# Optimization experiments

Hardware: AMD Instinct MI355X
Metric: run time of the kernel (lower is better)

The kernel has to match this reference:

```python
import jax, jax.numpy as jnp
import numpy as np

NB, NLOC, NALL, NNEI = 1, 4096, 6144, 64
N_EDGE, N_ANGLE, A_SEL = 262144, 409600, 10
N_DIM, E_DIM, A_DIM, AXIS = 128, 64, 32, 4
SEL_REDUCE = 10.0


def _lin_params(key, din, dout):
    k1, k2 = jax.random.split(key)
    W = jax.random.normal(k1, (din, dout), jnp.float32) / np.float32(np.sqrt(din))
    b = jax.random.normal(k2, (dout,), jnp.float32) * 0.01
    return W, b


def setup_inputs():
    key = jax.random.key(0)
    ks = jax.random.split(key, 20)
    inp = {}
    inp["node_ebd_ext"] = jax.random.normal(ks[0], (NB, NALL, N_DIM), jnp.float32)
    inp["edge_ebd"] = jax.random.normal(ks[1], (N_EDGE, E_DIM), jnp.float32)
    inp["h2"] = jax.random.normal(ks[2], (N_EDGE, 3), jnp.float32)
    inp["angle_ebd"] = jax.random.normal(ks[3], (N_ANGLE, A_DIM), jnp.float32)
    inp["nlist"] = jax.random.randint(ks[4], (NB, NLOC, NNEI), 0, NALL)
    inp["nlist_mask"] = jnp.ones((NB, NLOC, NNEI), jnp.bool_)
    inp["sw"] = jax.random.uniform(ks[5], (N_EDGE,), jnp.float32)
    inp["a_nlist"] = jax.random.randint(ks[6], (NB, NLOC, A_SEL), 0, NALL)
    inp["a_nlist_mask"] = jnp.ones((NB, NLOC, A_SEL), jnp.bool_)
    inp["a_sw"] = jax.random.uniform(ks[7], (N_ANGLE,), jnp.float32)
    n2e = jax.random.randint(ks[8], (N_EDGE,), 0, NB * NLOC)
    n_ext2e = jax.random.randint(ks[9], (N_EDGE,), 0, NB * NALL)
    inp["edge_index"] = jnp.stack([n2e, n_ext2e])
    n2a = jax.random.randint(ks[10], (N_ANGLE,), 0, NB * NLOC)
    eij2a = jax.random.randint(ks[11], (N_ANGLE,), 0, N_EDGE)
    eik2a = jax.random.randint(ks[12], (N_ANGLE,), 0, N_EDGE)
    inp["angle_index"] = jnp.stack([n2a, eij2a, eik2a])
    sym_dim = (N_DIM + E_DIM) * AXIS          # 768
    edge_info_dim = 2 * N_DIM + E_DIM         # 320
    angle_dim = A_DIM + N_DIM + 2 * E_DIM     # 288
    inp["W_node_self"], inp["b_node_self"] = _lin_params(ks[13], N_DIM, N_DIM)
    inp["W_node_sym"], inp["b_node_sym"] = _lin_params(ks[14], sym_dim, N_DIM)
    inp["W_node_edge"], inp["b_node_edge"] = _lin_params(ks[15], edge_info_dim, N_DIM)
    inp["W_edge_self"], inp["b_edge_self"] = _lin_params(ks[16], edge_info_dim, E_DIM)
    inp["W_edge_angle1"], inp["b_edge_angle1"] = _lin_params(ks[17], angle_dim, E_DIM)
    inp["W_edge_angle2"], inp["b_edge_angle2"] = _lin_params(ks[18], E_DIM, E_DIM)
    inp["W_angle_self"], inp["b_angle_self"] = _lin_params(ks[19], angle_dim, A_DIM)
    inp["n_res0"] = jnp.full((N_DIM,), 0.1, jnp.float32)
    inp["n_res1"] = jnp.full((N_DIM,), 0.1, jnp.float32)
    inp["n_res2"] = jnp.full((N_DIM,), 0.1, jnp.float32)
    inp["e_res0"] = jnp.full((E_DIM,), 0.1, jnp.float32)
    inp["e_res1"] = jnp.full((E_DIM,), 0.1, jnp.float32)
    inp["a_res0"] = jnp.full((A_DIM,), 0.1, jnp.float32)
    return inp


def reference(node_ebd_ext, edge_ebd, h2, angle_ebd, nlist, nlist_mask, sw,
              a_nlist, a_nlist_mask, a_sw, edge_index, angle_index,
              W_node_self, b_node_self, W_node_sym, b_node_sym,
              W_node_edge, b_node_edge, W_edge_self, b_edge_self,
              W_edge_angle1, b_edge_angle1, W_edge_angle2, b_edge_angle2,
              W_angle_self, b_angle_self,
              n_res0, n_res1, n_res2, e_res0, e_res1, a_res0):
    act = jax.nn.silu
    nb, nloc, nnei = nlist.shape
    n_dim = node_ebd_ext.shape[-1]
    n_edge = h2.shape[0]
    dyn_e_sel = nnei / SEL_REDUCE
    dyn_a_sel = a_nlist.shape[-1] / SEL_REDUCE
    node_ebd = node_ebd_ext[:, :nloc]
    n2e, n_ext2e = edge_index[0], edge_index[1]
    n2a, eij2a, eik2a = angle_index[0], angle_index[1], angle_index[2]
    nei_node_ebd = node_ebd_ext.reshape(-1, n_dim)[n_ext2e]  # [n_edge, n_dim]
    node_self = act(node_ebd @ W_node_self + b_node_self)

    def sym_op(flat_ebd):
        # symmetrization: outer(h2, sw*ebd) scattered to owners, then grrg
        d = flat_ebd.shape[-1]
        w = flat_ebd * sw[:, None]
        h2g2 = jax.ops.segment_sum(
            (h2[:, :, None] * w[:, None, :]).reshape(n_edge, 3 * d),
            n2e, num_segments=nb * nloc)
        h2g2 = h2g2.reshape(nb, nloc, 3, d) * (dyn_e_sel ** -0.5)
        m = h2g2[..., :AXIS]  # [nb, nloc, 3, axis]
        g = jnp.einsum('blxa,blxd->blad', m, h2g2) / 3.0
        return g.reshape(nb, nloc, AXIS * d)

    sym_edge = sym_op(edge_ebd)
    sym_node = sym_op(nei_node_ebd)
    node_sym = act(jnp.concatenate([sym_edge, sym_node], -1) @ W_node_sym + b_node_sym)
    node_i = node_ebd.reshape(-1, n_dim)[n2e]
    edge_info = jnp.concatenate([node_i, nei_node_ebd, edge_ebd], -1)  # [n_edge, 320]
    node_edge_update = act(edge_info @ W_node_edge + b_node_edge) * sw[:, None]
    node_edge_msg = jax.ops.segment_sum(node_edge_update, n2e, num_segments=nb * nloc).reshape(nb, nloc, -1) / dyn_e_sel
    n_updated = node_ebd + n_res0 * node_self + n_res1 * node_sym + n_res2 * node_edge_msg
    edge_self = act(edge_info @ W_edge_self + b_edge_self)
    node_for_angle = node_ebd.reshape(-1, n_dim)[n2a]
    edge_ik = edge_ebd[eik2a]
    edge_ij = edge_ebd[eij2a]
    angle_info = jnp.concatenate([angle_ebd, node_for_angle, edge_ik, edge_ij], -1)  # [n_angle, 288]
    edge_angle = act(angle_info @ W_edge_angle1 + b_edge_angle1)
    reduced = jax.ops.segment_sum(edge_angle * a_sw[:, None], eij2a, num_segments=n_edge) / (dyn_a_sel ** 0.5)
    edge_angle_msg = act(reduced @ W_edge_angle2 + b_edge_angle2)
    e_updated = edge_ebd + e_res0 * edge_self + e_res1 * edge_angle_msg
    angle_self = act(angle_info @ W_angle_self + b_angle_self)
    a_updated = angle_ebd + a_res0 * angle_self
    return (n_updated, e_updated, a_updated)
```

## Files before the change

### kernel.cpp

```cpp
#include <hip/hip_runtime.h>
#include <hip/hip_bf16.h>

#define NLOC_   4096
#define NALL_   6144
#define NEDGE_  262144
#define NANGLE_ 409600

typedef __bf16 bf16x8 __attribute__((ext_vector_type(8)));
typedef float  f32x4  __attribute__((ext_vector_type(4)));
typedef unsigned short u16;

__device__ __forceinline__ float silu_(float x){ return x / (1.0f + __expf(-x)); }

__device__ __forceinline__ u16 f2bu(float f){
    union { float f; unsigned u; } v; v.f = f;
    unsigned r = v.u + 0x7fffu + ((v.u >> 16) & 1u);
    return (u16)(r >> 16);
}
__device__ __forceinline__ float bu2f(u16 b){
    union { unsigned u; float f; } v; v.u = ((unsigned)b) << 16; return v.f;
}
__device__ __forceinline__ void st_bf16x4(u16* dst, float4 v){
    unsigned lo = (unsigned)f2bu(v.x) | ((unsigned)f2bu(v.y) << 16);
    unsigned hi = (unsigned)f2bu(v.z) | ((unsigned)f2bu(v.w) << 16);
    *reinterpret_cast<uint2*>(dst) = make_uint2(lo, hi);
}

__global__ __launch_bounds__(256) void k_mega_prep(
    const float* __restrict__ Wne, const float* __restrict__ Wes,
    const float* __restrict__ W1,  const float* __restrict__ WA,
    const float* __restrict__ W2,  const float* __restrict__ Wsym,
    const float* __restrict__ Wns,
    const float* __restrict__ node_ext, const float* __restrict__ edge_ebd,
    const float* __restrict__ angle_ebd,
    const int* __restrict__ n2e, const int* __restrict__ eij2a,
    u16* __restrict__ WTe, u16* __restrict__ WTa, u16* __restrict__ WT2,
    u16* __restrict__ WsymT, u16* __restrict__ WnsT,
    u16* __restrict__ NB, u16* __restrict__ EB, u16* __restrict__ AB,
    int* __restrict__ cnt, int* __restrict__ cnt2)
{
    const int b = blockIdx.x, tid = threadIdx.x;
    if (b < 812) {
        int i = b*256 + tid;
        if (i < 61440) {
            int r = i/320, c = i - r*320;
            WTe[i] = f2bu(r < 128 ? Wne[c*128 + r] : Wes[c*64 + (r-128)]);
        } else if (i < 89088) {
            int j = i - 61440; int r = j/288, c = j - r*288;
            WTa[j] = f2bu(r < 64 ? W1[c*64 + r] : WA[c*32 + (r-64)]);
        } else if (i < 93184) {
            int j = i - 89088; int r = j >> 6, c = j & 63;
            WT2[j] = f2bu(W2[c*64 + r]);
        } else if (i < 191488) {
            int j = i - 93184; int r = j/768, c = j - r*768;
            WsymT[j] = f2bu(Wsym[c*128 + r]);
        } else {
            int j = i - 191488; int r = j >> 7, c = j & 127;
            WnsT[j] = f2bu(Wns[c*128 + r]);
        }
    } else if (b < 1580) {
        int i = (b - 812)*256 + tid;
        float4 v = ((const float4*)node_ext)[i];
        st_bf16x4(&NB[(size_t)i*4], v);
    } else if (b < 3628) {
        for (int i = (b - 1580)*256 + tid; i < NEDGE_*64/4; i += 2048*256) {
            float4 v = ((const float4*)edge_ebd)[i];
            st_bf16x4(&EB[(size_t)i*4], v);
        }
    } else if (b < 5676) {
        for (int i = (b - 3628)*256 + tid; i < NANGLE_*32/4; i += 2048*256) {
            float4 v = ((const float4*)angle_ebd)[i];
            st_bf16x4(&AB[(size_t)i*4], v);
        }
    } else if (b < 6700) {
        int e = (b - 5676)*256 + tid;
        atomicAdd(&cnt[n2e[e]], 1);
    } else {
        int a = (b - 6700)*256 + tid;
        atomicAdd(&cnt2[eij2a[a]], 1);
    }
}

__global__ __launch_bounds__(256) void k_scan_misc(
    const int* __restrict__ cnt, int* __restrict__ off, int* __restrict__ cursor,
    const int* __restrict__ cnt2, int* __restrict__ bsum,
    const u16* __restrict__ NB, const u16* __restrict__ WTe,
    float* __restrict__ nconst)
{
    __shared__ __align__(16) u16 sN[64][136];
    int* wa = (int*)&sN[0][0];
    const int b = blockIdx.x, t = threadIdx.x;

    if (b == 0) {
        int v[16]; int s = 0;
        #pragma unroll
        for (int k = 0; k < 16; ++k) { v[k] = s; s += cnt[16*t + k]; }
        wa[t] = s;
        __syncthreads();
        for (int d = 1; d < 256; d <<= 1) {
            int x = wa[t];
            int y = (t >= d) ? wa[t-d] : 0;
            __syncthreads();
            wa[t] = x + y;
            __syncthreads();
        }
        int excl = (t == 0) ? 0 : wa[t-1];
        #pragma unroll
        for (int k = 0; k < 16; ++k) {
            off[16*t + k]    = excl + v[k];
            cursor[16*t + k] = excl + v[k];
        }
        if (t == 255) off[4096] = excl + s;
    } else if (b <= 256) {
        int bb = b - 1;
        int4 v = ((const int4*)cnt2)[bb*256 + t];
        wa[t] = v.x + v.y + v.z + v.w;
        __syncthreads();
        for (int d = 128; d > 0; d >>= 1) {
            if (t < d) wa[t] += wa[t+d];
            __syncthreads();
        }
        if (t == 0) bsum[bb] = wa[0];
    } else {
        const int e0 = (b - 257) * 64;
        #pragma unroll
        for (int f = t; f < 1024; f += 256) {
            int r = f >> 4, c = f & 15;
            *(uint4*)&sN[r][8*c] = ((const uint4*)&NB[(size_t)(e0 + r)*128])[c];
        }
        __syncthreads();
        const int w = t >> 6, l = t & 63;
        const int lr = l & 15, hq = l >> 4, lk = hq * 8;
        f32x4 acc[4][3] = {};
        #pragma unroll
        for (int kk = 0; kk < 4; ++kk) {
            bf16x8 a[4], bb[3];
            #pragma unroll
            for (int m = 0; m < 4; ++m)
                a[m] = *(const bf16x8*)&sN[16*m + lr][kk*32 + lk];
            #pragma unroll
            for (int nf = 0; nf < 3; ++nf)
                bb[nf] = *(const bf16x8*)&WTe[(size_t)(48*w + 16*nf + lr)*320 + kk*32 + lk];
            #pragma unroll
            for (int m = 0; m < 4; ++m)
                #pragma unroll
                for (int nf = 0; nf < 3; ++nf)
                    acc[m][nf] = __builtin_amdgcn_mfma_f32_16x16x32_bf16(a[m], bb[nf], acc[m][nf], 0, 0, 0);
        }
        #pragma unroll
        for (int nf = 0; nf < 3; ++nf) {
            int c = 48*w + 16*nf + lr;
            #pragma unroll
            for (int m = 0; m < 4; ++m)
                #pragma unroll
                for (int j = 0; j < 4; ++j) {
                    int r = 16*m + 4*hq + j;
                    nconst[(size_t)(e0 + r)*192 + c] = acc[m][nf][j];
                }
        }
    }
}

__global__ void k_scan2b(const int* __restrict__ bsum, int* __restrict__ boff)
{
    __shared__ int wa[256];
    int t = threadIdx.x;
    wa[t] = bsum[t];
    __syncthreads();
    for (int d = 1; d < 256; d <<= 1) {
        int x = wa[t];
        int y = (t >= d) ? wa[t-d] : 0;
        __syncthreads();
        wa[t] = x + y;
        __syncthreads();
    }
    boff[t] = (t == 0) ? 0 : wa[t-1];
}

__global__ void k_scan2c(const int* __restrict__ cnt2, const int* __restrict__ boff,
                         int* __restrict__ off2, int* __restrict__ cursor2)
{
    __shared__ int wa[256];
    int b = blockIdx.x, t = threadIdx.x;
    int4 v = ((const int4*)cnt2)[b*256 + t];
    int s1 = v.x, s2 = s1 + v.y, s3 = s2 + v.z, s4 = s3 + v.w;
    wa[t] = s4;
    __syncthreads();
    for (int d = 1; d < 256; d <<= 1) {
        int x = wa[t];
        int y = (t >= d) ? wa[t-d] : 0;
        __syncthreads();
        wa[t] = x + y;
        __syncthreads();
    }
    int base = boff[b] + ((t == 0) ? 0 : wa[t-1]);
    int i = (b*256 + t)*4;
    off2[i]   = base;      cursor2[i]   = base;
    off2[i+1] = base + s1; cursor2[i+1] = base + s1;
    off2[i+2] = base + s2; cursor2[i+2] = base + s2;
    off2[i+3] = base + s3; cursor2[i+3] = base + s3;
    if (b == 255 && t == 255) off2[NEDGE_] = NANGLE_;
}

__global__ void k_fill2(const int* __restrict__ n2e, int* __restrict__ cursor,
                        int* __restrict__ csr,
                        const int* __restrict__ eij2a, int* __restrict__ cursor2,
                        int* __restrict__ rank2)
{
    int b = blockIdx.x;
    if (b < 1024) {
        int e = b*256 + threadIdx.x;
        int pos = atomicAdd(&cursor[n2e[e]], 1);
        csr[pos] = e;
    } else {
        int a = (b - 1024)*256 + threadIdx.x;
        int pos = atomicAdd(&cursor2[eij2a[a]], 1);
        rank2[a] = pos;
    }
}

__global__ __launch_bounds__(256, 4) void k_edge_flat(
    const u16* __restrict__ NB, const u16* __restrict__ EB,
    const float* __restrict__ h2, const float* __restrict__ sw,
    const int* __restrict__ n2e, const int* __restrict__ n_ext2e,
    const int* __restrict__ csr,
    const u16* __restrict__ WTe, const float* __restrict__ nconst,
    const float* __restrict__ bne, const float* __restrict__ bes,
    float* __restrict__ msg,
    float* __restrict__ h2g2_e, float* __restrict__ h2g2_n,
    u16* __restrict__ eselfO)
{
    __shared__ __align__(16) u16 sA[64][200];
    __shared__ float sH[4][576];
    __shared__ int   s_eid[64];
    __shared__ int   s_node[64];
    __shared__ int   s_g[64];
    __shared__ float s_sw[64];
    __shared__ float s_h2[64][3];
    __shared__ int   s_segstart[65];
    __shared__ int   s_nseg;

    const int tid = threadIdx.x;
    const int w  = tid >> 6, l = tid & 63;
    const int lr = l & 15, hq = l >> 4, lk = hq * 8;
    const int base = blockIdx.x * 64;

    if (tid < 64) {
        int e = csr[base + tid];
        s_eid[tid]  = e;
        s_node[tid] = n2e[e];
        s_g[tid]    = n_ext2e[e];
        s_sw[tid]   = sw[e];
        s_h2[tid][0] = h2[e*3];
        s_h2[tid][1] = h2[e*3+1];
        s_h2[tid][2] = h2[e*3+2];
    }
    __syncthreads();

    if (tid < 64) {
        bool flag = (tid == 0) || (s_node[tid] != s_node[tid-1]);
        unsigned long long mask = __ballot(flag);
        if (flag) {
            int sid = __popcll(mask & ((1ull << tid) - 1ull));
            s_segstart[sid] = tid;
        }
        if (tid == 0) {
            int ns = __popcll(mask);
            s_nseg = ns;
            s_segstart[ns] = 64;
        }
    }

    #pragma unroll
    for (int f = tid; f < 1024; f += 256) {
        int r = f >> 4, c = f & 15;
        *(uint4*)&sA[r][8*c] = ((const uint4*)&NB[(size_t)s_g[r]*128])[c];
    }
    #pragma unroll
    for (int f = tid; f < 512; f += 256) {
        int r = f >> 3, c = f & 7;
        *(uint4*)&sA[r][128 + 8*c] = ((const uint4*)&EB[(size_t)s_eid[r]*64])[c];
    }
    __syncthreads();

    float bias[3];
    int   cful[3];
    #pragma unroll
    for (int nf = 0; nf < 3; ++nf) {
        int c = 48*w + 16*nf + lr;
        cful[nf] = c;
        bias[nf] = (c < 128) ? bne[c] : bes[c-128];
    }

    f32x4 acc[4][3] = {};
    #pragma unroll
    for (int kk = 0; kk < 6; ++kk) {
        bf16x8 a[4], b[3];
        #pragma unroll
        for (int m = 0; m < 4; ++m)
            a[m] = *(const bf16x8*)&sA[16*m + lr][kk*32 + lk];
        #pragma unroll
        for (int nf = 0; nf < 3; ++nf)
            b[nf] = *(const bf16x8*)&WTe[(size_t)cful[nf]*320 + 128 + kk*32 + lk];
        #pragma unroll
        for (int m = 0; m < 4; ++m)
            #pragma unroll
            for (int nf = 0; nf < 3; ++nf)
                acc[m][nf] = __builtin_amdgcn_mfma_f32_16x16x32_bf16(a[m], b[nf], acc[m][nf], 0, 0, 0);
    }

    #pragma unroll
    for (int nf = 0; nf < 3; ++nf) {
        int c = cful[nf];
        if (c < 128) {
            #pragma unroll
            for (int m = 0; m < 4; ++m)
                #pragma unroll
                for (int j = 0; j < 4; ++j) {
                    int r = 16*m + 4*hq + j;
                    float ncv = nconst[(size_t)s_node[r]*192 + c];
                    acc[m][nf][j] = silu_(acc[m][nf][j] + ncv + bias[nf]) * s_sw[r];
                }
        } else {
            int c2 = c - 128;
            #pragma unroll
            for (int m = 0; m < 4; ++m)
                #pragma unroll
                for (int j = 0; j < 4; ++j) {
                    int r = 16*m + 4*hq + j;
                    float ncv = nconst[(size_t)s_node[r]*192 + c];
                    eselfO[(size_t)s_eid[r]*64 + c2] =
                        f2bu(silu_(acc[m][nf][j] + ncv + bias[nf]));
                }
        }
    }

    const int nseg = s_nseg;
    for (int s = 0; s < nseg; ++s) {
        int rs = s_segstart[s], re = s_segstart[s+1];
        int nd = s_node[rs];
        #pragma unroll
        for (int nf = 0; nf < 3; ++nf) {
            if (cful[nf] >= 128) continue;
            float v = 0.f;
            #pragma unroll
            for (int m = 0; m < 4; ++m)
                #pragma unroll
                for (int j = 0; j < 4; ++j) {
                    int r = 16*m + 4*hq + j;
                    v += (r >= rs && r < re) ? acc[m][nf][j] : 0.f;
                }
            v += __shfl_xor(v, 16);
            v += __shfl_xor(v, 32);
            if (hq == 0) atomicAdd(&msg[(size_t)nd*128 + cful[nf]], v);
        }
    }

    for (int s = 0; s < nseg; ++s) {
        int rs = s_segstart[s], re = s_segstart[s+1];
        int nd = s_node[rs];
        int lo = max(16*w, rs), hi = min(16*w + 16, re);
        float hacc[9] = {0.f,0.f,0.f,0.f,0.f,0.f,0.f,0.f,0.f};
        for (int r = lo; r < hi; ++r) {
            float swv = s_sw[r];
            float s0 = s_h2[r][0] * swv;
            float s1 = s_h2[r][1] * swv;
            float s2 = s_h2[r][2] * swv;
            float eb = bu2f(sA[r][128 + l]);
            float n0 = bu2f(sA[r][l]);
            float n1 = bu2f(sA[r][64 + l]);
            hacc[0] = fmaf(s0, eb, hacc[0]);
            hacc[1] = fmaf(s1, eb, hacc[1]);
            hacc[2] = fmaf(s2, eb, hacc[2]);
            hacc[3] = fmaf(s0, n0, hacc[3]);
            hacc[4] = fmaf(s0, n1, hacc[4]);
            hacc[5] = fmaf(s1, n0, hacc[5]);
            hacc[6] = fmaf(s1, n1, hacc[6]);
            hacc[7] = fmaf(s2, n0, hacc[7]);
            hacc[8] = fmaf(s2, n1, hacc[8]);
        }
        #pragma unroll
        for (int q = 0; q < 3; ++q) sH[w][q*64 + l] = hacc[q];
        #pragma unroll
        for (int q = 0; q < 6; ++q) sH[w][192 + q*64 + l] = hacc[3+q];
        __syncthreads();
        for (int i = tid; i < 576; i += 256) {
            float v = sH[0][i] + sH[1][i] + sH[2][i] + sH[3][i];
            if (i < 192) atomicAdd(&h2g2_e[(size_t)nd*192 + i], v);
            else         atomicAdd(&h2g2_n[(size_t)nd*384 + (i - 192)], v);
        }
        __syncthreads();
    }
}

__global__ __launch_bounds__(256) void k_angle_mfma(
    const u16* __restrict__ NB, const u16* __restrict__ EB,
    const u16* __restrict__ AB, const float* __restrict__ a_sw,
    const int* __restrict__ n2a, const int* __restrict__ eij2a,
    const int* __restrict__ eik2a, const int* __restrict__ rank2,
    const u16* __restrict__ WTa,
    const float* __restrict__ b1, const float* __restrict__ bA,
    const float* __restrict__ a_res0,
    u16* __restrict__ ea, float* __restrict__ a_out)
{
    __shared__ __align__(16) u16 sA[32][296];
    __shared__ __align__(16) u16 sEA[32][64];
    __shared__ int s_na[32], s_ij[32], s_ik[32], s_rk[32];
    __shared__ float s_asw[32];
    const int tid = threadIdx.x;
    const int a0 = blockIdx.x * 32;

    if (tid < 32) {
        s_na[tid] = n2a[a0 + tid];
        s_ij[tid] = eij2a[a0 + tid];
        s_ik[tid] = eik2a[a0 + tid];
        s_rk[tid] = rank2[a0 + tid];
        s_asw[tid] = a_sw[a0 + tid];
    }
    __syncthreads();

    if (tid < 128) {
        int r = tid >> 2, c = tid & 3;
        *(uint4*)&sA[r][8*c] = ((const uint4*)&AB[(size_t)(a0 + r)*32])[c];
    }
    #pragma unroll
    for (int f = tid; f < 512; f += 256) {
        int r = f >> 4, c = f & 15;
        *(uint4*)&sA[r][32 + 8*c] = ((const uint4*)&NB[(size_t)s_na[r]*128])[c];
    }
    {
        int r = tid >> 3, c = tid & 7;
        *(uint4*)&sA[r][160 + 8*c] = ((const uint4*)&EB[(size_t)s_ik[r]*64])[c];
        *(uint4*)&sA[r][224 + 8*c] = ((const uint4*)&EB[(size_t)s_ij[r]*64])[c];
    }
    __syncthreads();

    const int w = tid >> 6, l = tid & 63;
    const int lr = l & 15, hq = l >> 4, lk = hq * 8;
    const int mrow  = (w & 1) * 16;
    const int nbase = (w >> 1) * 48;

    f32x4 acc[3] = {};
    #pragma unroll
    for (int kk = 0; kk < 9; ++kk) {
        bf16x8 a = *(const bf16x8*)&sA[mrow + lr][kk*32 + lk];
        #pragma unroll
        for (int nf = 0; nf < 3; ++nf) {
            bf16x8 b = *(const bf16x8*)&WTa[(size_t)(nbase + 16*nf + lr)*288 + kk*32 + lk];
            acc[nf] = __builtin_amdgcn_mfma_f32_16x16x32_bf16(a, b, acc[nf], 0, 0, 0);
        }
    }

    #pragma unroll
    for (int nf = 0; nf < 3; ++nf) {
        int c = nbase + 16*nf + lr;
        if (c < 64) {
            float bb = b1[c];
            #pragma unroll
            for (int j = 0; j < 4; ++j) {
                int r = mrow + 4*hq + j;
                sEA[r][c] = f2bu(silu_(acc[nf][j] + bb) * s_asw[r]);
            }
        } else {
            int c2 = c - 64;
            float bb = bA[c2], rr = a_res0[c2];
            #pragma unroll
            for (int j = 0; j < 4; ++j) {
                int r = mrow + 4*hq + j;
                size_t idx = (size_t)(a0 + r)*32 + c2;
                a_out[idx] = bu2f(sA[r][c2]) + rr * silu_(acc[nf][j] + bb);
            }
        }
    }
    __syncthreads();

    {
        int r = tid >> 3, c = tid & 7;
        *(uint4*)&ea[(size_t)s_rk[r]*64 + 8*c] = *(const uint4*)&sEA[r][8*c];
    }
}

__global__ __launch_bounds__(256) void k_fin(
    const u16* __restrict__ EB, const u16* __restrict__ eselfO,
    const u16* __restrict__ ea, const int* __restrict__ off2,
    const u16* __restrict__ WT2,
    const float* __restrict__ b2_, const float* __restrict__ er0,
    const float* __restrict__ er1,
    float* __restrict__ e_out,
    const float* __restrict__ h2g2_e, const float* __restrict__ h2g2_n,
    u16* __restrict__ symcB)
{
    __shared__ __align__(16) u16 sR[64][72];
    __shared__ __align__(16) u16 sE[64][72];
    __shared__ __align__(16) u16 sB[64][72];
    const int tid = threadIdx.x;
    const int blk = blockIdx.x;

    if (blk < 4096) {
        const int e0 = blk * 64;
        const int w = tid >> 6, l = tid & 63;

        #pragma unroll
        for (int f = tid; f < 512; f += 256) {
            int r = f >> 3, c = f & 7;
            *(uint4*)&sB[r][8*c] = ((const uint4*)&EB[(size_t)(e0 + r)*64])[c];
            *(uint4*)&sE[r][8*c] = ((const uint4*)&eselfO[(size_t)(e0 + r)*64])[c];
        }

        #pragma unroll
        for (int r16 = 0; r16 < 16; ++r16) {
            int r = w*16 + r16;
            int e = e0 + r;
            float s = 0.f;
            int jb = off2[e], je = off2[e+1];
            for (int j = jb; j < je; ++j)
                s += bu2f(ea[(size_t)j*64 + l]);
            sR[r][l] = f2bu(s);
        }
        __syncthreads();

        const int lr = l & 15, hq = l >> 4, lk = hq * 8;
        f32x4 acc[4] = {};
        #pragma unroll
        for (int kk = 0; kk < 2; ++kk) {
            bf16x8 b = *(const bf16x8*)&WT2[(size_t)(16*w + lr)*64 + kk*32 + lk];
            #pragma unroll
            for (int m = 0; m < 4; ++m) {
                bf16x8 a = *(const bf16x8*)&sR[16*m + lr][kk*32 + lk];
                acc[m] = __builtin_amdgcn_mfma_f32_16x16x32_bf16(a, b, acc[m], 0, 0, 0);
            }
        }
        int c = 16*w + lr;
        float bb = b2_[c], r0 = er0[c], r1 = er1[c];
        #pragma unroll
        for (int m = 0; m < 4; ++m)
            #pragma unroll
            for (int j = 0; j < 4; ++j) {
                int r = 16*m + 4*hq + j;
                size_t idx = (size_t)(e0 + r)*64 + c;
                e_out[idx] = bu2f(sB[r][c]) + r0 * bu2f(sE[r][c])
                           + r1 * silu_(acc[m][j] + bb);
            }
    } else {
        const int n = blk - 4096;
        float* he = (float*)&sR[0][0];
        float* hn = he + 192;
        for (int i = tid; i < 192; i += 256) he[i] = h2g2_e[(size_t)n*192 + i];
        for (int i = tid; i < 384; i += 256) hn[i] = h2g2_n[(size_t)n*384 + i];
        __syncthreads();
        const float SCALE = 1.0f / (6.4f * 3.0f);
        for (int i = tid; i < 768; i += 256) {
            float s;
            if (i < 256) {
                int a = i >> 6, j = i & 63;
                s = he[a]*he[j] + he[64+a]*he[64+j] + he[128+a]*he[128+j];
            } else {
                int i2 = i - 256;
                int a = i2 >> 7, j = i2 & 127;
                s = hn[a]*hn[j] + hn[128+a]*hn[128+j] + hn[256+a]*hn[256+j];
            }
            symcB[(size_t)n*768 + i] = f2bu(s * SCALE);
        }
    }
}

__global__ __launch_bounds__(256) void k_node_mfma(
    const u16* __restrict__ symcB, const u16* __restrict__ NB,
    const float* __restrict__ node_ext, const float* __restrict__ msg,
    const u16* __restrict__ WsymT, const u16* __restrict__ WnsT,
    const float* __restrict__ bns, const float* __restrict__ bsym,
    const float* __restrict__ nr0, const float* __restrict__ nr1,
    const float* __restrict__ nr2,
    float* __restrict__ n_out)
{
    __shared__ __align__(16) u16 sA[32][264];
    const int tid = threadIdx.x;
    const int n0 = blockIdx.x * 32;
    const int w = tid >> 6, l = tid & 63;
    const int lr = l & 15, hq = l >> 4, lk = hq * 8;

    f32x4 accY[2][2] = {};
    f32x4 accS[2][2] = {};

    for (int chunk = 0; chunk < 3; ++chunk) {
        __syncthreads();
        #pragma unroll
        for (int f = tid; f < 1024; f += 256) {
            int r = f >> 5, c = f & 31;
            *(uint4*)&sA[r][8*c] =
                ((const uint4*)&symcB[(size_t)(n0 + r)*768 + chunk*256])[c];
        }
        __syncthreads();
        #pragma unroll
        for (int kk = 0; kk < 8; ++kk) {
            bf16x8 a[2], b[2];
            #pragma unroll
            for (int m = 0; m < 2; ++m)
                a[m] = *(const bf16x8*)&sA[16*m + lr][kk*32 + lk];
            #pragma unroll
            for (int nf = 0; nf < 2; ++nf)
                b[nf] = *(const bf16x8*)&WsymT[(size_t)(32*w + 16*nf + lr)*768
                                               + chunk*256 + kk*32 + lk];
            #pragma unroll
            for (int m = 0; m < 2; ++m)
                #pragma unroll
                for (int nf = 0; nf < 2; ++nf)
                    accY[m][nf] = __builtin_amdgcn_mfma_f32_16x16x32_bf16(a[m], b[nf], accY[m][nf], 0, 0, 0);
        }
    }

    __syncthreads();
    #pragma unroll
    for (int f = tid; f < 512; f += 256) {
        int r = f >> 4, c = f & 15;
        *(uint4*)&sA[r][8*c] = ((const uint4*)&NB[(size_t)(n0 + r)*128])[c];
    }
    __syncthreads();
    #pragma unroll
    for (int kk = 0; kk < 4; ++kk) {
        bf16x8 a[2], b[2];
        #pragma unroll
        for (int m = 0; m < 2; ++m)
            a[m] = *(const bf16x8*)&sA[16*m + lr][kk*32 + lk];
        #pragma unroll
        for (int nf = 0; nf < 2; ++nf)
            b[nf] = *(const bf16x8*)&WnsT[(size_t)(32*w + 16*nf + lr)*128 + kk*32 + lk];
        #pragma unroll
        for (int m = 0; m < 2; ++m)
            #pragma unroll
            for (int nf = 0; nf < 2; ++nf)
                accS[m][nf] = __builtin_amdgcn_mfma_f32_16x16x32_bf16(a[m], b[nf], accS[m][nf], 0, 0, 0);
    }

    #pragma unroll
    for (int nf = 0; nf < 2; ++nf) {
        int c = 32*w + 16*nf + lr;
        float bS = bns[c], bY = bsym[c];
        float r0 = nr0[c], r1 = nr1[c], r2 = nr2[c];
        #pragma unroll
        for (int m = 0; m < 2; ++m)
            #pragma unroll
            for (int j = 0; j < 4; ++j) {
                int r = 16*m + 4*hq + j;
                size_t idx = (size_t)(n0 + r)*128 + c;
                float self_ = silu_(accS[m][nf][j] + bS);
                float sym_  = silu_(accY[m][nf][j] + bY);
                n_out[idx] = node_ext[idx] + r0*self_ + r1*sym_
                           + r2 * msg[idx] * (1.0f / 6.4f);
            }
    }
}

extern "C" void kernel_launch(void* const* d_in, const int* in_sizes, int n_in,
                              void* d_out, int out_size, void* d_ws, size_t ws_size,
                              hipStream_t stream)
{
    const float* node_ext  = (const float*)d_in[0];
    const float* edge_ebd  = (const float*)d_in[1];
    const float* h2        = (const float*)d_in[2];
    const float* angle_ebd = (const float*)d_in[3];
    const float* sw        = (const float*)d_in[6];
    const float* a_sw      = (const float*)d_in[9];
    const int*  edge_index  = (const int*)d_in[10];
    const int*  angle_index = (const int*)d_in[11];
    const int* n2e     = edge_index;
    const int* n_ext2e = edge_index + NEDGE_;
    const int* n2a     = angle_index;
    const int* eij2a   = angle_index + NANGLE_;
    const int* eik2a   = angle_index + 2*NANGLE_;

    const float* Wns  = (const float*)d_in[12];
    const float* bns  = (const float*)d_in[13];
    const float* Wsym = (const float*)d_in[14];
    const float* bsym = (const float*)d_in[15];
    const float* Wne  = (const float*)d_in[16];
    const float* bne  = (const float*)d_in[17];
    const float* Wes  = (const float*)d_in[18];
    const float* bes  = (const float*)d_in[19];
    const float* W1   = (const float*)d_in[20];
    const float* b1   = (const float*)d_in[21];
    const float* W2   = (const float*)d_in[22];
    const float* b2_  = (const float*)d_in[23];
    const float* WA   = (const float*)d_in[24];
    const float* bA   = (const float*)d_in[25];
    const float* nr0  = (const float*)d_in[26];
    const float* nr1  = (const float*)d_in[27];
    const float* nr2  = (const float*)d_in[28];
    const float* er0  = (const float*)d_in[29];
    const float* er1  = (const float*)d_in[30];
    const float* ar0  = (const float*)d_in[31];

    char* wsp = (char*)d_ws;
    u16*   ea      = (u16*)wsp;    wsp += (size_t)NANGLE_ * 64 * 2;
    u16*   EB      = (u16*)wsp;    wsp += (size_t)NEDGE_ * 64 * 2;
    u16*   NB      = (u16*)wsp;    wsp += (size_t)NALL_ * 128 * 2;
    u16*   AB      = (u16*)wsp;    wsp += (size_t)NANGLE_ * 32 * 2;
    u16*   eselfO  = (u16*)wsp;    wsp += (size_t)NEDGE_ * 64 * 2;
    u16*   symcB   = (u16*)wsp;    wsp += (size_t)NLOC_ * 768 * 2;
    int*   cnt     = (int*)wsp;    wsp += 4096 * 4;
    int*   cnt2    = (int*)wsp;    wsp += (size_t)NEDGE_ * 4;
    float* msg     = (float*)wsp;  wsp += (size_t)NLOC_ * 128 * 4;
    float* h2g2_e  = (float*)wsp;  wsp += (size_t)NLOC_ * 192 * 4;
    float* h2g2_n  = (float*)wsp;  wsp += (size_t)NLOC_ * 384 * 4;
    size_t zero_bytes = 4096*4 + (size_t)NEDGE_*4 + (size_t)NLOC_*128*4
                      + (size_t)NLOC_*192*4 + (size_t)NLOC_*384*4;
    int*   off     = (int*)wsp;    wsp += 4104 * 4;
    int*   cursor  = (int*)wsp;    wsp += 4096 * 4;
    int*   csr     = (int*)wsp;    wsp += (size_t)NEDGE_ * 4;
    int*   off2    = (int*)wsp;    wsp += ((size_t)NEDGE_ + 16) * 4;
    int*   cursor2 = (int*)wsp;    wsp += (size_t)NEDGE_ * 4;
    int*   bsum    = (int*)wsp;    wsp += 256 * 4;
    int*   boff    = (int*)wsp;    wsp += 256 * 4;
    int*   rank2   = (int*)wsp;    wsp += (size_t)NANGLE_ * 4;
    float* nconst  = (float*)wsp;  wsp += (size_t)NLOC_ * 192 * 4;
    u16*   WTe     = (u16*)wsp;    wsp += 192 * 320 * 2;
    u16*   WTa     = (u16*)wsp;    wsp += 96 * 288 * 2;
    u16*   WT2     = (u16*)wsp;    wsp += 64 * 64 * 2;
    u16*   WsymT   = (u16*)wsp;    wsp += 128 * 768 * 2;
    u16*   WnsT    = (u16*)wsp;    wsp += 128 * 128 * 2;

    hipMemsetAsync(cnt, 0, zero_bytes, stream);

    float* n_out = (float*)d_out;
    float* e_out = n_out + (size_t)NLOC_ * 128;
    float* a_out = e_out + (size_t)NEDGE_ * 64;

    k_mega_prep <<<8300, 256, 0, stream>>>(Wne, Wes, W1, WA, W2, Wsym, Wns,
                                           node_ext, edge_ebd, angle_ebd,
                                           n2e, eij2a,
                                           WTe, WTa, WT2, WsymT, WnsT,
                                           NB, EB, AB, cnt, cnt2);
    k_scan_misc <<<321, 256, 0, stream>>>(cnt, off, cursor, cnt2, bsum,
                                          NB, WTe, nconst);
    k_scan2b <<<1, 256, 0, stream>>>(bsum, boff);
    k_scan2c <<<256, 256, 0, stream>>>(cnt2, boff, off2, cursor2);
    k_fill2  <<<2624, 256, 0, stream>>>(n2e, cursor, csr, eij2a, cursor2, rank2);

    k_edge_flat <<<NEDGE_/64, 256, 0, stream>>>(NB, EB, h2, sw, n2e, n_ext2e, csr,
                                                WTe, nconst, bne, bes,
                                                msg, h2g2_e, h2g2_n, eselfO);
    k_angle_mfma <<<NANGLE_/32, 256, 0, stream>>>(NB, EB, AB, a_sw,
                                                  n2a, eij2a, eik2a, rank2,
                                                  WTa, b1, bA, ar0, ea, a_out);
    k_fin <<<8192, 256, 0, stream>>>(EB, eselfO, ea, off2, WT2, b2_, er0, er1,
                                     e_out, h2g2_e, h2g2_n, symcB);
    k_node_mfma <<<NLOC_/32, 256, 0, stream>>>(symcB, NB, node_ext, msg,
                                               WsymT, WnsT, bns, bsym,
                                               nr0, nr1, nr2, n_out);
}
```

Measured before the change: 423.8 us.

## Precompute per-node angle projection and iterate angles in CSR-sorted order

The node part of the angle linear layer (node_for_angle @ W[32:160]) is now computed once per local node (4096x96) in the scan kernel and stored in nconstA. The angle kernel then only gathers the angle and edge features (K=160 instead of 288) and adds the per-node constant before the activation. Angles are also processed in eij-sorted CSR order, so the ea stores become contiguous, but the angle_ebd reads and a_out writes are now scattered. This trades the per-angle 128-wide node gather and its MFMA work for an extra small GEMM and per-element gathers of nconstA.

```diff
diff --git a/kernel.cpp b/kernel.cpp
--- a/kernel.cpp
+++ b/kernel.cpp
@@ -34,8 +34,8 @@
     const float* __restrict__ node_ext, const float* __restrict__ edge_ebd,
     const float* __restrict__ angle_ebd,
     const int* __restrict__ n2e, const int* __restrict__ eij2a,
-    u16* __restrict__ WTe, u16* __restrict__ WTa, u16* __restrict__ WT2,
-    u16* __restrict__ WsymT, u16* __restrict__ WnsT,
+    u16* __restrict__ WTe, u16* __restrict__ WTa2, u16* __restrict__ WTaN,
+    u16* __restrict__ WT2, u16* __restrict__ WsymT, u16* __restrict__ WnsT,
     u16* __restrict__ NB, u16* __restrict__ EB, u16* __restrict__ AB,
     int* __restrict__ cnt, int* __restrict__ cnt2)
 {
@@ -45,9 +45,14 @@
         if (i < 61440) {
             int r = i/320, c = i - r*320;
             WTe[i] = f2bu(r < 128 ? Wne[c*128 + r] : Wes[c*64 + (r-128)]);
+        } else if (i < 76800) {
+            int j = i - 61440; int r = j/160, c2 = j - r*160;
+            int k = (c2 < 32) ? c2 : c2 + 128;
+            WTa2[j] = f2bu(r < 64 ? W1[k*64 + r] : WA[k*32 + (r-64)]);
         } else if (i < 89088) {
-            int j = i - 61440; int r = j/288, c = j - r*288;
-            WTa[j] = f2bu(r < 64 ? W1[c*64 + r] : WA[c*32 + (r-64)]);
+            int j = i - 76800; int r = j >> 7, c2 = j & 127;
+            int k = c2 + 32;
+            WTaN[j] = f2bu(r < 64 ? W1[k*64 + r] : WA[k*32 + (r-64)]);
         } else if (i < 93184) {
             int j = i - 89088; int r = j >> 6, c = j & 63;
             WT2[j] = f2bu(W2[c*64 + r]);
@@ -85,7 +90,8 @@
     const int* __restrict__ cnt, int* __restrict__ off, int* __restrict__ cursor,
     const int* __restrict__ cnt2, int* __restrict__ bsum,
     const u16* __restrict__ NB, const u16* __restrict__ WTe,
-    float* __restrict__ nconst)
+    const u16* __restrict__ WTaN,
+    float* __restrict__ nconst, float* __restrict__ nconstA)
 {
     __shared__ __align__(16) u16 sN[64][136];
     int* wa = (int*)&sN[0][0];
@@ -121,7 +127,7 @@
             __syncthreads();
         }
         if (t == 0) bsum[bb] = wa[0];
-    } else {
+    } else if (b <= 320) {
         const int e0 = (b - 257) * 64;
         #pragma unroll
         for (int f = t; f < 1024; f += 256) {
@@ -157,6 +163,35 @@
                     int r = 16*m + 4*hq + j;
                     nconst[(size_t)(e0 + r)*192 + c] = acc[m][nf][j];
                 }
+        }
+    } else {
+        const int n0 = (b - 321) * 64;
+        #pragma unroll
+        for (int f = t; f < 1024; f += 256) {
+            int r = f >> 4, c = f & 15;
+            *(uint4*)&sN[r][8*c] = ((const uint4*)&NB[(size_t)(n0 + r)*128])[c];
+        }
+        __syncthreads();
+        const int w = t >> 6, l = t & 63;
+        const int lr = l & 15, hq = l >> 4, lk = hq * 8;
+        f32x4 acc[6] = {};
+        #pragma unroll
+        for (int kk = 0; kk < 4; ++kk) {
+            bf16x8 a = *(const bf16x8*)&sN[16*w + lr][kk*32 + lk];
+            #pragma unroll
+            for (int nf = 0; nf < 6; ++nf) {
+                bf16x8 bb = *(const bf16x8*)&WTaN[(size_t)(16*nf + lr)*128 + kk*32 + lk];
+                acc[nf] = __builtin_amdgcn_mfma_f32_16x16x32_bf16(a, bb, acc[nf], 0, 0, 0);
+            }
+        }
+        #pragma unroll
+        for (int nf = 0; nf < 6; ++nf) {
+            int c = 16*nf + lr;
+            #pragma unroll
+            for (int j = 0; j < 4; ++j) {
+                int r = 16*w + 4*hq + j;
+                nconstA[(size_t)(n0 + r)*96 + c] = acc[nf][j];
+            }
         }
     }
 }
@@ -205,7 +240,7 @@
 __global__ void k_fill2(const int* __restrict__ n2e, int* __restrict__ cursor,
                         int* __restrict__ csr,
                         const int* __restrict__ eij2a, int* __restrict__ cursor2,
-                        int* __restrict__ rank2)
+                        int* __restrict__ csr2)
 {
     int b = blockIdx.x;
     if (b < 1024) {
@@ -215,7 +250,7 @@
     } else {
         int a = (b - 1024)*256 + threadIdx.x;
         int pos = atomicAdd(&cursor2[eij2a[a]], 1);
-        rank2[a] = pos;
+        csr2[pos] = a;
     }
 }
 
@@ -394,44 +429,40 @@
 }
 
 __global__ __launch_bounds__(256) void k_angle_mfma(
-    const u16* __restrict__ NB, const u16* __restrict__ EB,
-    const u16* __restrict__ AB, const float* __restrict__ a_sw,
+    const u16* __restrict__ EB, const u16* __restrict__ AB,
+    const float* __restrict__ a_sw,
     const int* __restrict__ n2a, const int* __restrict__ eij2a,
-    const int* __restrict__ eik2a, const int* __restrict__ rank2,
-    const u16* __restrict__ WTa,
+    const int* __restrict__ eik2a, const int* __restrict__ csr2,
+    const u16* __restrict__ WTa2, const float* __restrict__ nconstA,
     const float* __restrict__ b1, const float* __restrict__ bA,
     const float* __restrict__ a_res0,
     u16* __restrict__ ea, float* __restrict__ a_out)
 {
-    __shared__ __align__(16) u16 sA[32][296];
+    __shared__ __align__(16) u16 sA[32][168];
     __shared__ __align__(16) u16 sEA[32][64];
-    __shared__ int s_na[32], s_ij[32], s_ik[32], s_rk[32];
+    __shared__ int s_a[32], s_nd[32], s_ij[32], s_ik[32];
     __shared__ float s_asw[32];
     const int tid = threadIdx.x;
-    const int a0 = blockIdx.x * 32;
+    const int p0 = blockIdx.x * 32;
 
     if (tid < 32) {
-        s_na[tid] = n2a[a0 + tid];
-        s_ij[tid] = eij2a[a0 + tid];
-        s_ik[tid] = eik2a[a0 + tid];
-        s_rk[tid] = rank2[a0 + tid];
-        s_asw[tid] = a_sw[a0 + tid];
+        int a = csr2[p0 + tid];
+        s_a[tid]  = a;
+        s_nd[tid] = n2a[a];
+        s_ij[tid] = eij2a[a];
+        s_ik[tid] = eik2a[a];
+        s_asw[tid] = a_sw[a];
     }
     __syncthreads();
 
     if (tid < 128) {
         int r = tid >> 2, c = tid & 3;
-        *(uint4*)&sA[r][8*c] = ((const uint4*)&AB[(size_t)(a0 + r)*32])[c];
-    }
-    #pragma unroll
-    for (int f = tid; f < 512; f += 256) {
-        int r = f >> 4, c = f & 15;
-        *(uint4*)&sA[r][32 + 8*c] = ((const uint4*)&NB[(size_t)s_na[r]*128])[c];
+        *(uint4*)&sA[r][8*c] = ((const uint4*)&AB[(size_t)s_a[r]*32])[c];
     }
     {
         int r = tid >> 3, c = tid & 7;
-        *(uint4*)&sA[r][160 + 8*c] = ((const uint4*)&EB[(size_t)s_ik[r]*64])[c];
-        *(uint4*)&sA[r][224 + 8*c] = ((const uint4*)&EB[(size_t)s_ij[r]*64])[c];
+        *(uint4*)&sA[r][32 + 8*c] = ((const uint4*)&EB[(size_t)s_ik[r]*64])[c];
+        *(uint4*)&sA[r][96 + 8*c] = ((const uint4*)&EB[(size_t)s_ij[r]*64])[c];
     }
     __syncthreads();
 
@@ -442,11 +473,11 @@
 
     f32x4 acc[3] = {};
     #pragma unroll
-    for (int kk = 0; kk < 9; ++kk) {
+    for (int kk = 0; kk < 5; ++kk) {
         bf16x8 a = *(const bf16x8*)&sA[mrow + lr][kk*32 + lk];
         #pragma unroll
         for (int nf = 0; nf < 3; ++nf) {
-            bf16x8 b = *(const bf16x8*)&WTa[(size_t)(nbase + 16*nf + lr)*288 + kk*32 + lk];
+            bf16x8 b = *(const bf16x8*)&WTa2[(size_t)(nbase + 16*nf + lr)*160 + kk*32 + lk];
             acc[nf] = __builtin_amdgcn_mfma_f32_16x16x32_bf16(a, b, acc[nf], 0, 0, 0);
         }
     }
@@ -459,7 +490,8 @@
             #pragma unroll
             for (int j = 0; j < 4; ++j) {
                 int r = mrow + 4*hq + j;
-                sEA[r][c] = f2bu(silu_(acc[nf][j] + bb) * s_asw[r]);
+                float nca = nconstA[(size_t)s_nd[r]*96 + c];
+                sEA[r][c] = f2bu(silu_(acc[nf][j] + nca + bb) * s_asw[r]);
             }
         } else {
             int c2 = c - 64;
@@ -467,8 +499,9 @@
             #pragma unroll
             for (int j = 0; j < 4; ++j) {
                 int r = mrow + 4*hq + j;
-                size_t idx = (size_t)(a0 + r)*32 + c2;
-                a_out[idx] = bu2f(sA[r][c2]) + rr * silu_(acc[nf][j] + bb);
+                float nca = nconstA[(size_t)s_nd[r]*96 + c];
+                a_out[(size_t)s_a[r]*32 + c2] =
+                    bu2f(sA[r][c2]) + rr * silu_(acc[nf][j] + nca + bb);
             }
         }
     }
@@ -476,7 +509,7 @@
 
     {
         int r = tid >> 3, c = tid & 7;
-        *(uint4*)&ea[(size_t)s_rk[r]*64 + 8*c] = *(const uint4*)&sEA[r][8*c];
+        *(uint4*)&ea[((size_t)(p0 + r))*64 + 8*c] = *(const uint4*)&sEA[r][8*c];
     }
 }
 
@@ -711,10 +744,12 @@
     int*   cursor2 = (int*)wsp;    wsp += (size_t)NEDGE_ * 4;
     int*   bsum    = (int*)wsp;    wsp += 256 * 4;
     int*   boff    = (int*)wsp;    wsp += 256 * 4;
-    int*   rank2   = (int*)wsp;    wsp += (size_t)NANGLE_ * 4;
+    int*   csr2    = (int*)wsp;    wsp += (size_t)NANGLE_ * 4;
     float* nconst  = (float*)wsp;  wsp += (size_t)NLOC_ * 192 * 4;
+    float* nconstA = (float*)wsp;  wsp += (size_t)NLOC_ * 96 * 4;
     u16*   WTe     = (u16*)wsp;    wsp += 192 * 320 * 2;
-    u16*   WTa     = (u16*)wsp;    wsp += 96 * 288 * 2;
+    u16*   WTa2    = (u16*)wsp;    wsp += 96 * 160 * 2;
+    u16*   WTaN    = (u16*)wsp;    wsp += 96 * 128 * 2;
     u16*   WT2     = (u16*)wsp;    wsp += 64 * 64 * 2;
     u16*   WsymT   = (u16*)wsp;    wsp += 128 * 768 * 2;
     u16*   WnsT    = (u16*)wsp;    wsp += 128 * 128 * 2;
@@ -728,20 +763,21 @@
     k_mega_prep <<<8300, 256, 0, stream>>>(Wne, Wes, W1, WA, W2, Wsym, Wns,
                                            node_ext, edge_ebd, angle_ebd,
                                            n2e, eij2a,
-                                           WTe, WTa, WT2, WsymT, WnsT,
+                                           WTe, WTa2, WTaN, WT2, WsymT, WnsT,
                                            NB, EB, AB, cnt, cnt2);
-    k_scan_misc <<<321, 256, 0, stream>>>(cnt, off, cursor, cnt2, bsum,
-                                          NB, WTe, nconst);
+    k_scan_misc <<<385, 256, 0, stream>>>(cnt, off, cursor, cnt2, bsum,
+                                          NB, WTe, WTaN, nconst, nconstA);
     k_scan2b <<<1, 256, 0, stream>>>(bsum, boff);
     k_scan2c <<<256, 256, 0, stream>>>(cnt2, boff, off2, cursor2);
-    k_fill2  <<<2624, 256, 0, stream>>>(n2e, cursor, csr, eij2a, cursor2, rank2);
+    k_fill2  <<<2624, 256, 0, stream>>>(n2e, cursor, csr, eij2a, cursor2, csr2);
 
     k_edge_flat <<<NEDGE_/64, 256, 0, stream>>>(NB, EB, h2, sw, n2e, n_ext2e, csr,
                                                 WTe, nconst, bne, bes,
                                                 msg, h2g2_e, h2g2_n, eselfO);
-    k_angle_mfma <<<NANGLE_/32, 256, 0, stream>>>(NB, EB, AB, a_sw,
-                                                  n2a, eij2a, eik2a, rank2,
-                                                  WTa, b1, bA, ar0, ea, a_out);
+    k_angle_mfma <<<NANGLE_/32, 256, 0, stream>>>(EB, AB, a_sw,
+                                                  n2a, eij2a, eik2a, csr2,
+                                                  WTa2, nconstA, b1, bA, ar0,
+                                                  ea, a_out);
     k_fin <<<8192, 256, 0, stream>>>(EB, eselfO, ea, off2, WT2, b2_, er0, er1,
                                      e_out, h2g2_e, h2g2_n, symcB);
     k_node_mfma <<<NLOC_/32, 256, 0, stream>>>(symcB, NB, node_ext, msg,
```

Result: no change. 422.6 us (-0.3%).
